# Kernel tuning notes

Measured on AMD Instinct MI355X. Metric: run time of the kernel, lower is better.

## Reference

```python
import jax, jax.numpy as jnp
import numpy as np

TOP_K = 2

def setup_inputs() -> dict:
    key = jax.random.key(0)
    kx, kg, k1, k2 = jax.random.split(key, 4)
    B, T, D, E, H = 4, 1024, 1024, 8, 2048
    x = jax.random.normal(kx, (B, T, D), dtype=jnp.float32)
    Wg = jax.random.normal(kg, (D, E), dtype=jnp.float32) * 0.02
    W1 = jax.random.normal(k1, (E, D, H), dtype=jnp.float32) * 0.02  # c_fc per expert
    W2 = jax.random.normal(k2, (E, H, D), dtype=jnp.float32) * 0.02  # c_proj per expert
    return {"x": x, "Wg": Wg, "W1": W1, "W2": W2}

def reference(x, Wg, W1, W2):
    B, T, D = x.shape
    E = W1.shape[0]
    # Router: softmax over experts, top-k, renormalize top-k weights
    logits = jnp.einsum('btd,de->bte', x, Wg)          # (B,T,E)
    probs = jax.nn.softmax(logits, axis=-1)
    top_w, top_i = jax.lax.top_k(probs, TOP_K)          # (B,T,K)
    top_w = top_w / (jnp.sum(top_w, axis=-1, keepdims=True) + 1e-8)
    # Combine weights per (token, expert): sum_k top_w[k] * one_hot(top_i[k])
    N = B * T
    oh = jax.nn.one_hot(top_i.reshape(N, TOP_K), E, dtype=x.dtype)   # (N,K,E)
    combine = jnp.sum(oh * top_w.reshape(N, TOP_K)[..., None], axis=1)  # (N,E)
    # Expert MLPs: relu(x W1)^2 W2, evaluated densely and combined (same math)
    xt = x.reshape(N, D)
    h = jnp.einsum('td,edh->teh', xt, W1)               # (N,E,H)
    h = jnp.square(jax.nn.relu(h))
    y = jnp.einsum('teh,ehd->ted', h, W2)               # (N,E,D)
    out = jnp.einsum('te,ted->td', combine, y)          # (N,D)
    return out.reshape(B, T, D)
```

## Files before the change

### kernel.cpp

```cpp
#include <hip/hip_runtime.h>
#include <hip/hip_bf16.h>
#include <stdint.h>

#define NTOK 4096
#define DD 1024
#define EE 8
#define HH 2048
#define BM 128
#define BN 128
#define BK 64
#define MAXRB 72
#define RPAD (MAXRB*BM)

typedef __attribute__((ext_vector_type(4))) float f32x4;
typedef __attribute__((ext_vector_type(8))) short bf16x8;

__device__ __forceinline__ void gload16(const void* g, void* l) {
  __builtin_amdgcn_global_load_lds((const __attribute__((address_space(1))) unsigned int*)g,
                                   (__attribute__((address_space(3))) unsigned int*)l, 16, 0, 0);
}

__global__ __launch_bounds__(256) void router_kernel(const float* __restrict__ x,
    const float* __restrict__ Wg, double* __restrict__ logitsD) {
  int t = blockIdx.x;
  int tid = threadIdx.x;
  const float* xr = x + (size_t)t * DD;
  double acc[EE];
  #pragma unroll
  for (int e = 0; e < EE; ++e) acc[e] = 0.0;
  #pragma unroll
  for (int i = 0; i < DD/256; ++i) {
    int d = tid + i*256;
    float xv = xr[d];
    float4 w0 = *(const float4*)(Wg + (size_t)d*EE);
    float4 w1 = *(const float4*)(Wg + (size_t)d*EE + 4);
    double xd = (double)xv;
    acc[0] += xd * (double)w0.x; acc[1] += xd * (double)w0.y;
    acc[2] += xd * (double)w0.z; acc[3] += xd * (double)w0.w;
    acc[4] += xd * (double)w1.x; acc[5] += xd * (double)w1.y;
    acc[6] += xd * (double)w1.z; acc[7] += xd * (double)w1.w;
  }
  #pragma unroll
  for (int e = 0; e < EE; ++e) {
    double v = acc[e];
    #pragma unroll
    for (int off = 32; off > 0; off >>= 1) v += __shfl_down(v, off, 64);
    acc[e] = v;
  }
  __shared__ double sAcc[4][EE];
  int lane = tid & 63, w = tid >> 6;
  if (lane == 0) {
    #pragma unroll
    for (int e = 0; e < EE; ++e) sAcc[w][e] = acc[e];
  }
  __syncthreads();
  if (tid < EE)
    logitsD[(size_t)t*EE + tid] = sAcc[0][tid] + sAcc[1][tid] + sAcc[2][tid] + sAcc[3][tid];
}

__global__ __launch_bounds__(256) void softtop_kernel(const double* __restrict__ logitsD,
    int* __restrict__ topE, float* __restrict__ topW, int* __restrict__ counts) {
  __shared__ int hist[EE];
  if (threadIdx.x < EE) hist[threadIdx.x] = 0;
  __syncthreads();
  int t = blockIdx.x * 256 + threadIdx.x;
  double s[EE];
  #pragma unroll
  for (int e = 0; e < EE; ++e) s[e] = logitsD[(size_t)t*EE + e];
  double mx = s[0];
  #pragma unroll
  for (int e = 1; e < EE; ++e) mx = fmax(mx, s[e]);
  double p[EE], Z = 0.0;
  #pragma unroll
  for (int e = 0; e < EE; ++e) { p[e] = exp(s[e] - mx); Z += p[e]; }
  #pragma unroll
  for (int e = 0; e < EE; ++e) p[e] /= Z;
  int i0 = 0;
  #pragma unroll
  for (int e = 1; e < EE; ++e) if (p[e] > p[i0]) i0 = e;
  int i1 = -1;
  #pragma unroll
  for (int e = 0; e < EE; ++e) { if (e == i0) continue; if (i1 < 0 || p[e] > p[i1]) i1 = e; }
  double sm = p[i0] + p[i1] + 1e-8;
  topE[t*2]   = i0; topE[t*2+1] = i1;
  topW[t*2]   = (float)(p[i0] / sm);
  topW[t*2+1] = (float)(p[i1] / sm);
  atomicAdd(&hist[i0], 1); atomicAdd(&hist[i1], 1);
  __syncthreads();
  if (threadIdx.x < EE) atomicAdd(&counts[threadIdx.x], hist[threadIdx.x]);
}

__global__ __launch_bounds__(1024) void assign_kernel(const int* __restrict__ counts,
    const int* __restrict__ topE, const float* __restrict__ topW,
    int* __restrict__ po, int* __restrict__ nRB, int* __restrict__ rbExpert,
    int* __restrict__ pairsTok, float* __restrict__ pairsW, int* __restrict__ slotOf) {
  __shared__ int base[EE];
  __shared__ int wcnt[16][EE];
  int tid = threadIdx.x, wv = tid >> 6, lane = tid & 63;
  if (tid == 0) {
    int off = 0;
    for (int e = 0; e < EE; ++e) {
      po[e] = off;
      off += ((counts[e] + BM - 1) / BM) * BM;
    }
    po[EE] = off;
    *nRB = off / BM;
    int rb = 0;
    for (int e = 0; e < EE; ++e) {
      int nb = (counts[e] + BM - 1) / BM;
      for (int b = 0; b < nb; ++b) rbExpert[rb++] = e;
    }
  }
  for (int i = tid; i < RPAD; i += 1024) pairsTok[i] = -1;
  __syncthreads();
  if (tid < EE) base[tid] = po[tid];
  __syncthreads();
  for (int it = 0; it < 2*NTOK/1024; ++it) {
    int p = it*1024 + tid;
    int e = topE[p];
    int myrank = 0;
    #pragma unroll
    for (int ee = 0; ee < EE; ++ee) {
      unsigned long long b = __ballot(e == ee);
      if (ee == e) myrank = __popcll(b & ((1ull << lane) - 1ull));
      if (lane == 0) wcnt[wv][ee] = __popcll(b);
    }
    __syncthreads();
    int wbase = 0;
    for (int w2 = 0; w2 < wv; ++w2) wbase += wcnt[w2][e];
    int slot = base[e] + wbase + myrank;
    pairsTok[slot] = p >> 1;
    pairsW[slot]   = topW[p];
    slotOf[p]      = slot;
    __syncthreads();
    if (tid < EE) {
      int s2 = 0;
      #pragma unroll
      for (int w2 = 0; w2 < 16; ++w2) s2 += wcnt[w2][tid];
      base[tid] += s2;
    }
    __syncthreads();
  }
}

__global__ __launch_bounds__(256) void gather_kernel(const float* __restrict__ x,
    const int* __restrict__ slotOf, __hip_bfloat16* __restrict__ Xg) {
  int t = blockIdx.x;
  int s0 = slotOf[2*t], s1 = slotOf[2*t+1];
  const float* xr = x + (size_t)t * DD;
  int i = threadIdx.x;
  float4 v = ((const float4*)xr)[i];
  ushort4 b;
  b.x = __bfloat16_as_ushort(__float2bfloat16(v.x));
  b.y = __bfloat16_as_ushort(__float2bfloat16(v.y));
  b.z = __bfloat16_as_ushort(__float2bfloat16(v.z));
  b.w = __bfloat16_as_ushort(__float2bfloat16(v.w));
  ((ushort4*)(Xg + (size_t)s0 * DD))[i] = b;
  ((ushort4*)(Xg + (size_t)s1 * DD))[i] = b;
}

__global__ __launch_bounds__(256) void transpose_conv_kernel(const float* __restrict__ in,
    __hip_bfloat16* __restrict__ out, int R, int C) {
  __shared__ __hip_bfloat16 tile[64][70];
  int tilesC = C >> 6;
  int tilesPerE = (R >> 6) * tilesC;
  int b = blockIdx.x;
  int e = b / tilesPerE;
  int rem = b % tilesPerE;
  int tr = rem / tilesC, tc = rem % tilesC;
  const float* src = in + (size_t)e * R * C + (size_t)(tr*64) * C + tc*64;
  int rr = threadIdx.x >> 4;
  int c4 = (threadIdx.x & 15) << 2;
  #pragma unroll
  for (int i = 0; i < 4; ++i) {
    int r = rr + (i << 4);
    float4 v = *(const float4*)(src + (size_t)r * C + c4);
    ushort4 u;
    u.x = __bfloat16_as_ushort(__float2bfloat16(v.x));
    u.y = __bfloat16_as_ushort(__float2bfloat16(v.y));
    u.z = __bfloat16_as_ushort(__float2bfloat16(v.z));
    u.w = __bfloat16_as_ushort(__float2bfloat16(v.w));
    *(ushort4*)&tile[r][c4] = u;
  }
  __syncthreads();
  __hip_bfloat16* dst = out + (size_t)e * R * C + (size_t)(tc*64) * R + tr*64;
  int orow = threadIdx.x >> 2;
  int seg  = (threadIdx.x & 3) << 4;
  bf16x8 w0, w1;
  #pragma unroll
  for (int j = 0; j < 8; ++j) w0[j] = (short)__bfloat16_as_ushort(tile[seg + j][orow]);
  #pragma unroll
  for (int j = 0; j < 8; ++j) w1[j] = (short)__bfloat16_as_ushort(tile[seg + 8 + j][orow]);
  *(bf16x8*)(dst + (size_t)orow * R + seg)     = w0;
  *(bf16x8*)(dst + (size_t)orow * R + seg + 8) = w1;
}

template<int EPI, int KDIM, int NTOT>
__global__ __launch_bounds__(256, 4)
void gemm_kernel(const __hip_bfloat16* __restrict__ A,
                 const __hip_bfloat16* __restrict__ Ball,
                 __hip_bfloat16* __restrict__ Cbf,
                 float* __restrict__ Cf,
                 const int* __restrict__ nRB,
                 const int* __restrict__ rbExpert,
                 const int* __restrict__ pairsTok,
                 const float* __restrict__ pairsW) {
  int nrb = *nRB;
  int cpx = (nrb + 7) >> 3;
  int bid = blockIdx.x;
  int xcd = bid & 7;
  int slot = bid >> 3;
  int lr = slot % 9;
  int nb = slot / 9;
  int rb = xcd * cpx + lr;
  if (lr >= cpx || rb >= nrb) return;
  int e = rbExpert[rb];
  const __hip_bfloat16* Ag = A + (size_t)rb * BM * KDIM;
  const __hip_bfloat16* Bg = Ball + (size_t)e * NTOT * KDIM + (size_t)nb * BN * KDIM;
  __shared__ __align__(16) __hip_bfloat16 As[BM*BK];
  __shared__ __align__(16) __hip_bfloat16 Bs[BN*BK];
  __shared__ int   sTok[BM];
  __shared__ float sW[BM];
  int tid = threadIdx.x;
  if (EPI == 1 && tid < BM) {
    sTok[tid] = pairsTok[rb*BM + tid];
    sW[tid]   = pairsW[rb*BM + tid];
  }
  int lane = tid & 63;
  int wid = tid >> 6;
  int wr = wid >> 1, wc = wid & 1;
  int l15 = lane & 15;
  int lhi = lane >> 4;
  f32x4 acc[4][4] = {};
  int srow  = tid >> 3;
  int scol8 = (tid & 7) * 8;
  for (int kt = 0; kt < KDIM / BK; ++kt) {
    #pragma unroll
    for (int i = 0; i < 4; ++i) {
      int r = srow + 32*i;
      int sc = scol8 ^ ((r & 7) << 3);
      gload16(Ag + (size_t)r * KDIM + kt*BK + sc, (char*)As + i*4096 + tid*16);
      gload16(Bg + (size_t)r * KDIM + kt*BK + sc, (char*)Bs + i*4096 + tid*16);
    }
    __syncthreads();
    #pragma unroll
    for (int kk = 0; kk < 2; ++kk) {
      bf16x8 af[4], bfr[4];
      int kb = kk*64 + lhi*16;
      #pragma unroll
      for (int m = 0; m < 4; ++m) {
        int row = wr*64 + m*16 + l15;
        af[m] = *(const bf16x8*)((const char*)As + row*128 + (kb ^ ((row & 7) << 4)));
      }
      #pragma unroll
      for (int n = 0; n < 4; ++n) {
        int row = wc*64 + n*16 + l15;
        bfr[n] = *(const bf16x8*)((const char*)Bs + row*128 + (kb ^ ((row & 7) << 4)));
      }
      #pragma unroll
      for (int m = 0; m < 4; ++m)
        #pragma unroll
        for (int n = 0; n < 4; ++n)
          acc[m][n] = __builtin_amdgcn_mfma_f32_16x16x32_bf16(af[m], bfr[n], acc[m][n], 0, 0, 0);
    }
    __syncthreads();
  }
  if (EPI == 0) {
    #pragma unroll
    for (int m = 0; m < 4; ++m) {
      int row = rb*BM + wr*64 + m*16 + lhi*4;
      #pragma unroll
      for (int n = 0; n < 4; ++n) {
        int col = nb*BN + wc*64 + n*16 + l15;
        #pragma unroll
        for (int j = 0; j < 4; ++j) {
          float v = fmaxf(acc[m][n][j], 0.0f);
          Cbf[(size_t)(row + j) * NTOT + col] = __float2bfloat16(v * v);
        }
      }
    }
  } else {
    #pragma unroll
    for (int m = 0; m < 4; ++m) {
      int rloc = wr*64 + m*16 + lhi*4;
      #pragma unroll
      for (int j = 0; j < 4; ++j) {
        int tok = sTok[rloc + j];
        if (tok < 0) continue;
        float w = sW[rloc + j];
        #pragma unroll
        for (int n = 0; n < 4; ++n) {
          int col = nb*BN + wc*64 + n*16 + l15;
          atomicAdd(Cf + (size_t)tok * NTOT + col, w * acc[m][n][j]);
        }
      }
    }
  }
}


extern "C" void kernel_launch(void* const* d_in, const int* in_sizes, int n_in,
                              void* d_out, int out_size, void* d_ws, size_t ws_size,
                              hipStream_t stream) {
  const float* x  = (const float*)d_in[0];
  const float* Wg = (const float*)d_in[1];
  const float* W1 = (const float*)d_in[2];
  const float* W2 = (const float*)d_in[3];
  float* out = (float*)d_out;
  char* ws = (char*)d_ws;

  int*   counts   = (int*)(ws + 0);
  int*   po       = (int*)(ws + 128);
  int*   nRB      = (int*)(ws + 192);
  int*   rbExpert = (int*)(ws + 256);
  int*   topE     = (int*)(ws + 1024);
  float* topW     = (float*)(ws + 40960);
  int*   pairsTok = (int*)(ws + 73728);
  float* pairsW   = (float*)(ws + 110592);
  int*   slotOf   = (int*)(ws + 147456);
  __hip_bfloat16* Xg   = (__hip_bfloat16*)(ws + 262144);
  __hip_bfloat16* Hbuf = (__hip_bfloat16*)(ws + 19136512);
  double* logitsD = (double*)(ws + 19136512);
  __hip_bfloat16* W1bT = (__hip_bfloat16*)(ws + 56885248);
  __hip_bfloat16* W2bT = (__hip_bfloat16*)(ws + 90439680);

  hipMemsetAsync(d_out, 0, (size_t)out_size * sizeof(float), stream);
  hipMemsetAsync(ws, 0, 128, stream);

  router_kernel<<<NTOK, 256, 0, stream>>>(x, Wg, logitsD);
  softtop_kernel<<<NTOK/256, 256, 0, stream>>>(logitsD, topE, topW, counts);
  assign_kernel<<<1, 1024, 0, stream>>>(counts, topE, topW, po, nRB, rbExpert,
                                        pairsTok, pairsW, slotOf);
  gather_kernel<<<NTOK, 256, 0, stream>>>(x, slotOf, Xg);
  transpose_conv_kernel<<<EE*(DD/64)*(HH/64), 256, 0, stream>>>(W1, W1bT, DD, HH);
  transpose_conv_kernel<<<EE*(HH/64)*(DD/64), 256, 0, stream>>>(W2, W2bT, HH, DD);

  gemm_kernel<0, DD, HH><<<8*9*(HH/BN), 256, 0, stream>>>(
      Xg, W1bT, Hbuf, nullptr, nRB, rbExpert, pairsTok, pairsW);
  gemm_kernel<1, HH, DD><<<8*9*(DD/BN), 256, 0, stream>>>(
      Hbuf, W2bT, nullptr, out, nRB, rbExpert, pairsTok, pairsW);
}
```

Before: 210.2 us.

## Fuse weight transposes into router and first GEMM launches to overlap work

Folds the W1 transpose/convert into the router launch, so the two run as one grid, and folds the W2 transpose/convert into the first expert GEMM launch. Independent work can then overlap and two kernel launches go away. The transpose is rewritten to pack bf16 pairs into 32-bit words through a padded shared tile with word-sized stores. The GEMM body becomes a device function using a byte shared buffer. The cost is that GEMM blocks now share launch slots and occupancy with transpose blocks, and shared memory is sized for the larger of the two roles.

```diff
diff --git a/kernel.cpp b/kernel.cpp
--- a/kernel.cpp
+++ b/kernel.cpp
@@ -11,6 +11,8 @@
 #define BK 64
 #define MAXRB 72
 #define RPAD (MAXRB*BM)
+#define GG1 (8*9*(HH/BN))
+#define GG2 (8*9*(DD/BN))
 
 typedef __attribute__((ext_vector_type(4))) float f32x4;
 typedef __attribute__((ext_vector_type(8))) short bf16x8;
@@ -20,42 +22,86 @@
                                    (__attribute__((address_space(3))) unsigned int*)l, 16, 0, 0);
 }
 
-__global__ __launch_bounds__(256) void router_kernel(const float* __restrict__ x,
-    const float* __restrict__ Wg, double* __restrict__ logitsD) {
-  int t = blockIdx.x;
+__device__ __forceinline__ void transpose_body(uint32_t (*T)[33],
+    const float* __restrict__ in, __hip_bfloat16* __restrict__ out,
+    int R, int C, int tb) {
+  int tilesC = C >> 6;
+  int tilesPerE = (R >> 6) * tilesC;
+  int e = tb / tilesPerE;
+  int rem = tb % tilesPerE;
+  int tr = rem / tilesC, tc = rem % tilesC;
+  const float* src = in + (size_t)e * R * C + (size_t)(tr*64) * C + tc*64;
   int tid = threadIdx.x;
-  const float* xr = x + (size_t)t * DD;
-  double acc[EE];
-  #pragma unroll
-  for (int e = 0; e < EE; ++e) acc[e] = 0.0;
-  #pragma unroll
-  for (int i = 0; i < DD/256; ++i) {
-    int d = tid + i*256;
-    float xv = xr[d];
-    float4 w0 = *(const float4*)(Wg + (size_t)d*EE);
-    float4 w1 = *(const float4*)(Wg + (size_t)d*EE + 4);
-    double xd = (double)xv;
-    acc[0] += xd * (double)w0.x; acc[1] += xd * (double)w0.y;
-    acc[2] += xd * (double)w0.z; acc[3] += xd * (double)w0.w;
-    acc[4] += xd * (double)w1.x; acc[5] += xd * (double)w1.y;
-    acc[6] += xd * (double)w1.z; acc[7] += xd * (double)w1.w;
-  }
-  #pragma unroll
-  for (int e = 0; e < EE; ++e) {
-    double v = acc[e];
-    #pragma unroll
-    for (int off = 32; off > 0; off >>= 1) v += __shfl_down(v, off, 64);
-    acc[e] = v;
-  }
-  __shared__ double sAcc[4][EE];
-  int lane = tid & 63, w = tid >> 6;
-  if (lane == 0) {
-    #pragma unroll
-    for (int e = 0; e < EE; ++e) sAcc[w][e] = acc[e];
-  }
-  __syncthreads();
-  if (tid < EE)
-    logitsD[(size_t)t*EE + tid] = sAcc[0][tid] + sAcc[1][tid] + sAcc[2][tid] + sAcc[3][tid];
+  int c0  = (tid & 31) * 2;
+  int r2b = tid >> 5;
+  #pragma unroll
+  for (int i = 0; i < 4; ++i) {
+    int r2 = r2b + 8*i;
+    const float* p0 = src + (size_t)(2*r2) * C + c0;
+    float2 a = *(const float2*)p0;
+    float2 b = *(const float2*)(p0 + C);
+    uint32_t u0 = ((uint32_t)__bfloat16_as_ushort(__float2bfloat16(b.x)) << 16)
+                |  (uint32_t)__bfloat16_as_ushort(__float2bfloat16(a.x));
+    uint32_t u1 = ((uint32_t)__bfloat16_as_ushort(__float2bfloat16(b.y)) << 16)
+                |  (uint32_t)__bfloat16_as_ushort(__float2bfloat16(a.y));
+    T[c0][r2]   = u0;
+    T[c0+1][r2] = u1;
+  }
+  __syncthreads();
+  __hip_bfloat16* dst = out + (size_t)e * R * C + (size_t)(tc*64) * R + tr*64;
+  int c  = tid >> 2;
+  int ch = (tid & 3) * 8;
+  uint32_t v[8];
+  #pragma unroll
+  for (int j = 0; j < 8; ++j) v[j] = T[c][ch + j];
+  uint32_t* dp = (uint32_t*)(dst + (size_t)c * R + ch*2);
+  #pragma unroll
+  for (int j = 0; j < 8; ++j) dp[j] = v[j];
+}
+
+__global__ __launch_bounds__(256) void mega_kernel(const float* __restrict__ x,
+    const float* __restrict__ Wg, double* __restrict__ logitsD,
+    const float* __restrict__ W1, __hip_bfloat16* __restrict__ W1bT) {
+  __shared__ __align__(16) char smem[8448];
+  int b = blockIdx.x;
+  if (b < NTOK) {
+    int t = b;
+    int tid = threadIdx.x;
+    const float* xr = x + (size_t)t * DD;
+    double acc[EE];
+    #pragma unroll
+    for (int e = 0; e < EE; ++e) acc[e] = 0.0;
+    #pragma unroll
+    for (int i = 0; i < DD/256; ++i) {
+      int d = tid + i*256;
+      float xv = xr[d];
+      float4 w0 = *(const float4*)(Wg + (size_t)d*EE);
+      float4 w1 = *(const float4*)(Wg + (size_t)d*EE + 4);
+      double xd = (double)xv;
+      acc[0] += xd * (double)w0.x; acc[1] += xd * (double)w0.y;
+      acc[2] += xd * (double)w0.z; acc[3] += xd * (double)w0.w;
+      acc[4] += xd * (double)w1.x; acc[5] += xd * (double)w1.y;
+      acc[6] += xd * (double)w1.z; acc[7] += xd * (double)w1.w;
+    }
+    #pragma unroll
+    for (int e = 0; e < EE; ++e) {
+      double v = acc[e];
+      #pragma unroll
+      for (int off = 32; off > 0; off >>= 1) v += __shfl_down(v, off, 64);
+      acc[e] = v;
+    }
+    double (*sAcc)[EE] = (double(*)[EE])smem;
+    int lane = tid & 63, w = tid >> 6;
+    if (lane == 0) {
+      #pragma unroll
+      for (int e = 0; e < EE; ++e) sAcc[w][e] = acc[e];
+    }
+    __syncthreads();
+    if (tid < EE)
+      logitsD[(size_t)t*EE + tid] = sAcc[0][tid] + sAcc[1][tid] + sAcc[2][tid] + sAcc[3][tid];
+  } else {
+    transpose_body((uint32_t(*)[33])smem, W1, W1bT, DD, HH, b - NTOK);
+  }
 }
 
 __global__ __launch_bounds__(256) void softtop_kernel(const double* __restrict__ logitsD,
@@ -159,55 +205,14 @@
   ((ushort4*)(Xg + (size_t)s1 * DD))[i] = b;
 }
 
-__global__ __launch_bounds__(256) void transpose_conv_kernel(const float* __restrict__ in,
-    __hip_bfloat16* __restrict__ out, int R, int C) {
-  __shared__ __hip_bfloat16 tile[64][70];
-  int tilesC = C >> 6;
-  int tilesPerE = (R >> 6) * tilesC;
-  int b = blockIdx.x;
-  int e = b / tilesPerE;
-  int rem = b % tilesPerE;
-  int tr = rem / tilesC, tc = rem % tilesC;
-  const float* src = in + (size_t)e * R * C + (size_t)(tr*64) * C + tc*64;
-  int rr = threadIdx.x >> 4;
-  int c4 = (threadIdx.x & 15) << 2;
-  #pragma unroll
-  for (int i = 0; i < 4; ++i) {
-    int r = rr + (i << 4);
-    float4 v = *(const float4*)(src + (size_t)r * C + c4);
-    ushort4 u;
-    u.x = __bfloat16_as_ushort(__float2bfloat16(v.x));
-    u.y = __bfloat16_as_ushort(__float2bfloat16(v.y));
-    u.z = __bfloat16_as_ushort(__float2bfloat16(v.z));
-    u.w = __bfloat16_as_ushort(__float2bfloat16(v.w));
-    *(ushort4*)&tile[r][c4] = u;
-  }
-  __syncthreads();
-  __hip_bfloat16* dst = out + (size_t)e * R * C + (size_t)(tc*64) * R + tr*64;
-  int orow = threadIdx.x >> 2;
-  int seg  = (threadIdx.x & 3) << 4;
-  bf16x8 w0, w1;
-  #pragma unroll
-  for (int j = 0; j < 8; ++j) w0[j] = (short)__bfloat16_as_ushort(tile[seg + j][orow]);
-  #pragma unroll
-  for (int j = 0; j < 8; ++j) w1[j] = (short)__bfloat16_as_ushort(tile[seg + 8 + j][orow]);
-  *(bf16x8*)(dst + (size_t)orow * R + seg)     = w0;
-  *(bf16x8*)(dst + (size_t)orow * R + seg + 8) = w1;
-}
-
 template<int EPI, int KDIM, int NTOT>
-__global__ __launch_bounds__(256, 4)
-void gemm_kernel(const __hip_bfloat16* __restrict__ A,
-                 const __hip_bfloat16* __restrict__ Ball,
-                 __hip_bfloat16* __restrict__ Cbf,
-                 float* __restrict__ Cf,
-                 const int* __restrict__ nRB,
-                 const int* __restrict__ rbExpert,
-                 const int* __restrict__ pairsTok,
-                 const float* __restrict__ pairsW) {
+__device__ __forceinline__ void gemm_body(char* smem, int bid,
+    const __hip_bfloat16* __restrict__ A, const __hip_bfloat16* __restrict__ Ball,
+    __hip_bfloat16* __restrict__ Cbf, float* __restrict__ Cf,
+    const int* __restrict__ nRB, const int* __restrict__ rbExpert,
+    const int* __restrict__ pairsTok, const float* __restrict__ pairsW) {
   int nrb = *nRB;
   int cpx = (nrb + 7) >> 3;
-  int bid = blockIdx.x;
   int xcd = bid & 7;
   int slot = bid >> 3;
   int lr = slot % 9;
@@ -217,10 +222,10 @@
   int e = rbExpert[rb];
   const __hip_bfloat16* Ag = A + (size_t)rb * BM * KDIM;
   const __hip_bfloat16* Bg = Ball + (size_t)e * NTOT * KDIM + (size_t)nb * BN * KDIM;
-  __shared__ __align__(16) __hip_bfloat16 As[BM*BK];
-  __shared__ __align__(16) __hip_bfloat16 Bs[BN*BK];
-  __shared__ int   sTok[BM];
-  __shared__ float sW[BM];
+  __hip_bfloat16* As = (__hip_bfloat16*)smem;
+  __hip_bfloat16* Bs = (__hip_bfloat16*)(smem + 16384);
+  int*   sTok = (int*)(smem + 32768);
+  float* sW   = (float*)(smem + 32768 + 512);
   int tid = threadIdx.x;
   if (EPI == 1 && tid < BM) {
     sTok[tid] = pairsTok[rb*BM + tid];
@@ -296,6 +301,34 @@
       }
     }
   }
+}
+
+__global__ __launch_bounds__(256, 4)
+void gemm1_fused(const __hip_bfloat16* __restrict__ Xg,
+                 const __hip_bfloat16* __restrict__ W1bT,
+                 __hip_bfloat16* __restrict__ Hbuf,
+                 const int* __restrict__ nRB, const int* __restrict__ rbExpert,
+                 const int* __restrict__ pairsTok, const float* __restrict__ pairsW,
+                 const float* __restrict__ W2, __hip_bfloat16* __restrict__ W2bT) {
+  __shared__ __align__(16) char smem[33*1024 + 1024];
+  int bid = blockIdx.x;
+  if (bid < GG1) {
+    gemm_body<0, DD, HH>(smem, bid, Xg, W1bT, Hbuf, nullptr,
+                         nRB, rbExpert, pairsTok, pairsW);
+  } else {
+    transpose_body((uint32_t(*)[33])smem, W2, W2bT, HH, DD, bid - GG1);
+  }
+}
+
+__global__ __launch_bounds__(256, 4)
+void gemm2_kernel(const __hip_bfloat16* __restrict__ Hbuf,
+                  const __hip_bfloat16* __restrict__ W2bT,
+                  float* __restrict__ out,
+                  const int* __restrict__ nRB, const int* __restrict__ rbExpert,
+                  const int* __restrict__ pairsTok, const float* __restrict__ pairsW) {
+  __shared__ __align__(16) char smem[33*1024 + 1024];
+  gemm_body<1, HH, DD>(smem, blockIdx.x, Hbuf, W2bT, nullptr, out,
+                       nRB, rbExpert, pairsTok, pairsW);
 }
 
 
@@ -327,16 +360,14 @@
   hipMemsetAsync(d_out, 0, (size_t)out_size * sizeof(float), stream);
   hipMemsetAsync(ws, 0, 128, stream);
 
-  router_kernel<<<NTOK, 256, 0, stream>>>(x, Wg, logitsD);
+  mega_kernel<<<NTOK + 4096, 256, 0, stream>>>(x, Wg, logitsD, W1, W1bT);
   softtop_kernel<<<NTOK/256, 256, 0, stream>>>(logitsD, topE, topW, counts);
   assign_kernel<<<1, 1024, 0, stream>>>(counts, topE, topW, po, nRB, rbExpert,
                                         pairsTok, pairsW, slotOf);
   gather_kernel<<<NTOK, 256, 0, stream>>>(x, slotOf, Xg);
-  transpose_conv_kernel<<<EE*(DD/64)*(HH/64), 256, 0, stream>>>(W1, W1bT, DD, HH);
-  transpose_conv_kernel<<<EE*(HH/64)*(DD/64), 256, 0, stream>>>(W2, W2bT, HH, DD);
-
-  gemm_kernel<0, DD, HH><<<8*9*(HH/BN), 256, 0, stream>>>(
-      Xg, W1bT, Hbuf, nullptr, nRB, rbExpert, pairsTok, pairsW);
-  gemm_kernel<1, HH, DD><<<8*9*(DD/BN), 256, 0, stream>>>(
-      Hbuf, W2bT, nullptr, out, nRB, rbExpert, pairsTok, pairsW);
-}
+
+  gemm1_fused<<<GG1 + 4096, 256, 0, stream>>>(Xg, W1bT, Hbuf, nRB, rbExpert,
+                                              pairsTok, pairsW, W2, W2bT);
+  gemm2_kernel<<<GG2, 256, 0, stream>>>(Hbuf, W2bT, out, nRB, rbExpert,
+                                        pairsTok, pairsW);
+}
```

Result: faster. 195.1 us (-7.2%).
